# Kernel optimization log

Hardware: AMD Instinct MI355X
Metric: run time of the kernel (lower is better)

Reference implementation:

```python
import jax, jax.numpy as jnp
import numpy as np

D_MODEL = 1024
N_HEADS = 16
D_HEAD = D_MODEL // N_HEADS
B, T = 2, 2048


def setup_inputs() -> dict:
    key = jax.random.key(0)
    ks = jax.random.split(key, 8)
    s = 1.0 / np.sqrt(D_MODEL)
    return {
        "x": jax.random.normal(ks[0], (B, T, D_MODEL), dtype=jnp.float32),
        "ln_g": jnp.ones((D_MODEL,), jnp.float32),
        "ln_b": jnp.zeros((D_MODEL,), jnp.float32),
        "w_qkv": jax.random.normal(ks[1], (D_MODEL, 3 * D_MODEL), jnp.float32) * s,
        "b_qkv": jnp.zeros((3 * D_MODEL,), jnp.float32),
        "w_gate": jax.random.normal(ks[2], (D_MODEL, D_MODEL), jnp.float32) * s,
        "b_gate": jnp.zeros((D_MODEL,), jnp.float32),
        "w_proj": jax.random.normal(ks[3], (D_MODEL, D_MODEL), jnp.float32) * s,
        "b_proj": jnp.zeros((D_MODEL,), jnp.float32),
    }


def reference(x, ln_g, ln_b, w_qkv, b_qkv, w_gate, b_gate, w_proj, b_proj):
    Bb, Tt, Dd = x.shape
    H, dh = N_HEADS, D_HEAD

    # LayerNorm (eps=1e-5, torch default)
    mu = jnp.mean(x, axis=-1, keepdims=True)
    var = jnp.mean((x - mu) ** 2, axis=-1, keepdims=True)
    x_norm = (x - mu) / jnp.sqrt(var + 1e-5) * ln_g + ln_b

    qkv = x_norm @ w_qkv + b_qkv
    q, k, v = jnp.split(qkv, 3, axis=-1)

    # concept gate on the RAW input x (not x_norm), normalized by its mean
    gate_sig = jax.nn.sigmoid(x @ w_gate + b_gate)
    gate_norm = gate_sig / (jnp.mean(gate_sig, axis=-1, keepdims=True) + 1e-5)
    q = q * gate_norm
    k = k * gate_norm

    # [B,T,D] -> [B,H,T,dh]
    def to_heads(t):
        return t.reshape(Bb, Tt, H, dh).transpose(0, 2, 1, 3)

    q, k, v = to_heads(q), to_heads(k), to_heads(v)

    q = jax.nn.elu(q) + 1.0
    k = jax.nn.elu(k) + 1.0

    # materialized outer-product cumsum (faithful to source formulation)
    kv = jnp.einsum("bhtd,bhtm->bhtdm", k, v)          # [B,H,T,dh,dh]
    kv_cumsum = jnp.cumsum(kv, axis=2)
    out_num = jnp.einsum("bhtd,bhtdm->bhtm", q, kv_cumsum)
    k_cumsum = jnp.cumsum(k, axis=2)
    out_den = jnp.einsum("bhtd,bhtd->bht", q, k_cumsum)[..., None] + 1e-5
    out = out_num / out_den                              # [B,H,T,dh]

    out = out.transpose(0, 2, 1, 3).reshape(Bb, Tt, Dd)
    return out @ w_proj + b_proj
```

## Files before the change

### kernel.cpp

```cpp
#include <hip/hip_runtime.h>
#include <math.h>

constexpr int D      = 1024;
constexpr int H      = 16;
constexpr int DH     = 64;
constexpr int Bb     = 2;
constexpr int T      = 2048;
constexpr int BT     = Bb * T;
constexpr int CHUNK  = 64;
constexpr int NC     = T / CHUNK;
constexpr int LS     = 72;

typedef __attribute__((ext_vector_type(8))) short bf16x8;
typedef __attribute__((ext_vector_type(4))) float f32x4;

#define GLOAD_LDS16(gp, lp) \
    __builtin_amdgcn_global_load_lds((const __attribute__((address_space(1))) void*)(gp), \
                                     (__attribute__((address_space(3))) void*)(lp), 16, 0, 0)

__device__ __forceinline__ short to_bf16(float f) {
    unsigned u = __float_as_uint(f);
    unsigned r = (u + 0x7fffu + ((u >> 16) & 1u)) >> 16;
    return (short)r;
}
__device__ __forceinline__ float bf2f(short s) {
    return __uint_as_float(((unsigned)(unsigned short)s) << 16);
}

__device__ __forceinline__ float block_sum_256(float v, float* sbuf) {
    #pragma unroll
    for (int off = 32; off > 0; off >>= 1) v += __shfl_down(v, off, 64);
    int lane = threadIdx.x & 63;
    int wid  = threadIdx.x >> 6;
    if (lane == 0) sbuf[wid] = v;
    __syncthreads();
    float r = (threadIdx.x < 4) ? sbuf[threadIdx.x] : 0.0f;
    r += __shfl_down(r, 2, 64);
    r += __shfl_down(r, 1, 64);
    if (threadIdx.x == 0) sbuf[0] = r;
    __syncthreads();
    float outv = sbuf[0];
    __syncthreads();
    return outv;
}

__device__ __forceinline__ float elu1(float x) {
    return x > 0.0f ? x + 1.0f : __expf(x);
}

__global__ __launch_bounds__(256) void pre_kernel(const float* __restrict__ x,
                                                  const float* __restrict__ g,
                                                  const float* __restrict__ b,
                                                  const float* __restrict__ wq,
                                                  const float* __restrict__ wg,
                                                  const float* __restrict__ wp,
                                                  short* __restrict__ ynb,
                                                  short* __restrict__ xbb,
                                                  short* __restrict__ wTcomb,
                                                  short* __restrict__ wTp,
                                                  float* __restrict__ gmean) {
    __shared__ float sbuf[4];
    __shared__ short tile[32][33];
    int bid = blockIdx.x;
    if (bid < BT) {
        int row = bid;
        if (threadIdx.x == 0) gmean[row] = 0.0f;
        const float* xr = x + (size_t)row * D;
        int c = threadIdx.x * 4;
        float4 xv = *(const float4*)(xr + c);
        float mu = block_sum_256(xv.x + xv.y + xv.z + xv.w, sbuf) * (1.0f / D);
        float d0 = xv.x - mu, d1 = xv.y - mu, d2 = xv.z - mu, d3 = xv.w - mu;
        float var = block_sum_256(d0*d0 + d1*d1 + d2*d2 + d3*d3, sbuf) * (1.0f / D);
        float rstd = rsqrtf(var + 1e-5f);
        float4 gv = *(const float4*)(g + c);
        float4 bv = *(const float4*)(b + c);
        short4 o, xo;
        o.x = to_bf16(d0 * rstd * gv.x + bv.x);
        o.y = to_bf16(d1 * rstd * gv.y + bv.y);
        o.z = to_bf16(d2 * rstd * gv.z + bv.z);
        o.w = to_bf16(d3 * rstd * gv.w + bv.w);
        xo.x = to_bf16(xv.x); xo.y = to_bf16(xv.y);
        xo.z = to_bf16(xv.z); xo.w = to_bf16(xv.w);
        *(short4*)(ynb + (size_t)row * D + c) = o;
        *(short4*)(xbb + (size_t)row * D + c) = xo;
    } else {
        int t2 = bid - BT;
        const float* W; short* Wt; int N; int t;
        if (t2 < 3072)      { W = wq; Wt = wTcomb;                       N = 3072; t = t2; }
        else if (t2 < 4096) { W = wg; Wt = wTcomb + (size_t)3072 * 1024; N = 1024; t = t2 - 3072; }
        else                { W = wp; Wt = wTp;                          N = 1024; t = t2 - 4096; }
        int ntiles = N >> 5;
        int nb = (t % ntiles) * 32, kb = (t / ntiles) * 32;
        int tx = threadIdx.x & 31, ty = threadIdx.x >> 5;
        #pragma unroll
        for (int i = 0; i < 4; ++i) {
            int k = kb + ty + i * 8;
            tile[ty + i * 8][tx] = to_bf16(W[(size_t)k * N + nb + tx]);
        }
        __syncthreads();
        #pragma unroll
        for (int i = 0; i < 4; ++i) {
            int n = nb + ty + i * 8;
            Wt[(size_t)n * 1024 + kb + tx] = tile[tx][ty + i * 8];
        }
    }
}

#define SWZ(os) ((os) ^ ((((os) >> 6) & 3) << 3))
#define BARX() __builtin_amdgcn_s_barrier()
#define LGKM0() asm volatile("s_waitcnt lgkmcnt(0)" ::: "memory")
#define VMW(n) asm volatile("s_waitcnt vmcnt(" #n ")" ::: "memory")
#define MEMFENCE() asm volatile("" ::: "memory")

#define STG(Mp, rb, t, kc, isB) do {                                                       \
    short* _b = ldsbuf + ((((t) & 1)) << 15) + (((((isB) << 1) | (kc))) << 13) + wid * 1024; \
    const short* _g = (Mp) + (size_t)((rb) + wid * 32 + s_r) * 1024 + (t) * 64 + (kc) * 32 + s_c; \
    GLOAD_LDS16(_g, _b);                                                                   \
    GLOAD_LDS16(_g + (size_t)16 * 1024, _b + 512);                                         \
} while (0)

#define FRAGA(t, kc, mi) (*(const bf16x8*)(ldsbuf + (((t) & 1) << 15) + ((kc) << 13) + \
    SWZ((wm * 128 + (mi) * 16 + fr) * 32 + fk)))
#define FRAGB(t, kc, ni) (*(const bf16x8*)(ldsbuf + (((t) & 1) << 15) + ((2 + (kc)) << 13) + \
    SWZ((wn * 64 + (ni) * 16 + fr) * 32 + fk)))

#define GROUP(t, S1, S2, S3, S4, W2, W4) do {                                              \
    bf16x8 af[8], bq[4];                                                                   \
                                                                    \
    _Pragma("unroll") for (int mi = 0; mi < 8; ++mi) af[mi] = FRAGA(t, 0, mi);             \
    bq[0] = FRAGB(t, 0, 0); bq[1] = FRAGB(t, 0, 1);                                        \
    if (S1) STG(Wt, col0, (t) + 1, 1, 1);                                                  \
    BARX(); LGKM0();                                                                       \
    __builtin_amdgcn_s_setprio(1);                                                         \
    _Pragma("unroll") for (int mi = 0; mi < 8; ++mi) {                                     \
        acc[mi][0] = __builtin_amdgcn_mfma_f32_16x16x32_bf16(af[mi], bq[0], acc[mi][0], 0, 0, 0); \
        acc[mi][1] = __builtin_amdgcn_mfma_f32_16x16x32_bf16(af[mi], bq[1], acc[mi][1], 0, 0, 0); \
    }                                                                                      \
    __builtin_amdgcn_s_setprio(0);                                                         \
    BARX();                                                                                \
                                                                    \
    bq[2] = FRAGB(t, 0, 2); bq[3] = FRAGB(t, 0, 3);                                        \
    if (S2) STG(Ap, row0, (t) + 2, 0, 0);                                                  \
    BARX(); LGKM0();                                                                       \
    __builtin_amdgcn_s_setprio(1);                                                         \
    _Pragma("unroll") for (int mi = 0; mi < 8; ++mi) {                                     \
        acc[mi][2] = __builtin_amdgcn_mfma_f32_16x16x32_bf16(af[mi], bq[2], acc[mi][2], 0, 0, 0); \
        acc[mi][3] = __builtin_amdgcn_mfma_f32_16x16x32_bf16(af[mi], bq[3], acc[mi][3], 0, 0, 0); \
    }                                                                                      \
    __builtin_amdgcn_s_setprio(0);                                                         \
    W2; BARX();                                                                            \
                                                                    \
    _Pragma("unroll") for (int mi = 0; mi < 8; ++mi) af[mi] = FRAGA(t, 1, mi);             \
    bq[0] = FRAGB(t, 1, 0); bq[1] = FRAGB(t, 1, 1);                                        \
    if (S3) STG(Wt, col0, (t) + 2, 0, 1);                                                  \
    BARX(); LGKM0();                                                                       \
    __builtin_amdgcn_s_setprio(1);                                                         \
    _Pragma("unroll") for (int mi = 0; mi < 8; ++mi) {                                     \
        acc[mi][0] = __builtin_amdgcn_mfma_f32_16x16x32_bf16(af[mi], bq[0], acc[mi][0], 0, 0, 0); \
        acc[mi][1] = __builtin_amdgcn_mfma_f32_16x16x32_bf16(af[mi], bq[1], acc[mi][1], 0, 0, 0); \
    }                                                                                      \
    __builtin_amdgcn_s_setprio(0);                                                         \
    BARX();                                                                                \
                                                                    \
    bq[2] = FRAGB(t, 1, 2); bq[3] = FRAGB(t, 1, 3);                                        \
    if (S4) STG(Ap, row0, (t) + 2, 1, 0);                                                  \
    BARX(); LGKM0();                                                                       \
    __builtin_amdgcn_s_setprio(1);                                                         \
    _Pragma("unroll") for (int mi = 0; mi < 8; ++mi) {                                     \
        acc[mi][2] = __builtin_amdgcn_mfma_f32_16x16x32_bf16(af[mi], bq[2], acc[mi][2], 0, 0, 0); \
        acc[mi][3] = __builtin_amdgcn_mfma_f32_16x16x32_bf16(af[mi], bq[3], acc[mi][3], 0, 0, 0); \
    }                                                                                      \
    __builtin_amdgcn_s_setprio(0);                                                         \
    W4; BARX();                                                                            \
} while (0)

__global__ __launch_bounds__(512, 2) void gemm_fused_qkvgate(const short* __restrict__ xnb,
                                                             const short* __restrict__ xb,
                                                             const short* __restrict__ Wt,
                                                             const float* __restrict__ b_qkv,
                                                             const float* __restrict__ b_gate,
                                                             short* __restrict__ qkvb,
                                                             short* __restrict__ sigb,
                                                             float* __restrict__ gmean) {
    __shared__ short ldsbuf[2 * 32768];

    const int bid   = blockIdx.x;
    const int xcd   = bid & 7;
    const int local = bid >> 3;
    const int cx = xcd & 3, ry = xcd >> 2;
    const int bxx = cx * 4 + (local & 3);
    const int byy = ry * 8 + (local >> 2);
    const int row0 = byy * 256;
    const int col0 = bxx * 256;
    const bool isg = (col0 >= 3 * D);
    const short* Ap = isg ? xb : xnb;

    const int tid  = threadIdx.x;
    const int wid  = tid >> 6;
    const int lane = tid & 63;
    const int wm = wid >> 2;
    const int wn = wid & 3;
    const int fr = lane & 15;
    const int fk = (lane >> 4) * 8;

    const int s_r = lane >> 2;
    const int s_c = 8 * ((lane & 3) ^ ((lane >> 3) & 3));

    f32x4 acc[8][4] = {};

    STG(Ap, row0, 0, 0, 0); MEMFENCE();
    STG(Wt, col0, 0, 0, 1); MEMFENCE();
    STG(Ap, row0, 0, 1, 0); MEMFENCE();
    STG(Wt, col0, 0, 1, 1); MEMFENCE();
    STG(Ap, row0, 1, 0, 0); MEMFENCE();
    STG(Wt, col0, 1, 0, 1); MEMFENCE();
    STG(Ap, row0, 1, 1, 0);
    VMW(10);
    BARX();

    for (int t = 0; t < 14; ++t) GROUP(t, 1, 1, 1, 1, VMW(10), VMW(10));
    GROUP(14, 1, 0, 0, 0, VMW(8), VMW(4));
    GROUP(15, 0, 0, 0, 0, VMW(0), (void)0);

    const int ccol  = lane & 15;
    const int crow4 = (lane >> 4) * 4;
    if (!isg) {
        #pragma unroll
        for (int mi = 0; mi < 8; ++mi) {
            #pragma unroll
            for (int ni = 0; ni < 4; ++ni) {
                int col = col0 + wn * 64 + ni * 16 + ccol;
                float bv = b_qkv[col];
                #pragma unroll
                for (int r = 0; r < 4; ++r) {
                    int row = row0 + wm * 128 + mi * 16 + crow4 + r;
                    qkvb[(size_t)row * (3 * D) + col] = to_bf16(acc[mi][ni][r] + bv);
                }
            }
        }
    } else {
        #pragma unroll
        for (int mi = 0; mi < 8; ++mi) {
            #pragma unroll
            for (int r = 0; r < 4; ++r) {
                int lrow = row0 + wm * 128 + mi * 16 + crow4 + r;
                float psum = 0.0f;
                #pragma unroll
                for (int ni = 0; ni < 4; ++ni) {
                    int col = col0 + wn * 64 + ni * 16 + ccol - 3 * D;
                    float v = acc[mi][ni][r] + b_gate[col];
                    float sv = 1.0f / (1.0f + __expf(-v));
                    sigb[(size_t)lrow * D + col] = to_bf16(sv);
                    psum += sv;
                }
                psum += __shfl_xor(psum, 1, 64);
                psum += __shfl_xor(psum, 2, 64);
                psum += __shfl_xor(psum, 4, 64);
                psum += __shfl_xor(psum, 8, 64);
                if (ccol == 0) atomicAdd(&gmean[lrow], psum);
            }
        }
    }
}

__global__ __launch_bounds__(256) void chunk_state_mfma(const short* __restrict__ qkvb,
                                                        const short* __restrict__ sigb,
                                                        const float* __restrict__ gmean,
                                                        float* __restrict__ Sc,
                                                        float* __restrict__ zc) {
    __shared__ short Kt[DH * LS];
    __shared__ short Vt[DH * LS];
    int idx = blockIdx.x;
    int c = idx & (NC - 1), h = (idx >> 5) & (H - 1), b = idx >> 9;
    size_t bt0 = (size_t)b * T + c * CHUNK;
    const short* kbase = qkvb + bt0 * (3 * D) + D + h * DH;
    const short* vbase = kbase + D;
    const short* sbase = sigb + bt0 * D + h * DH;
    int tid = threadIdx.x;

    #pragma unroll
    for (int l = 0; l < 2; ++l) {
        int i  = tid + l * 256;
        int t  = i >> 3;
        int d8 = (i & 7) * 8;
        float invm = 1.0f / (gmean[bt0 + t] * (1.0f / D) + 1e-5f);
        bf16x8 kv = *(const bf16x8*)(kbase + (size_t)t * (3 * D) + d8);
        bf16x8 vv = *(const bf16x8*)(vbase + (size_t)t * (3 * D) + d8);
        bf16x8 sg = *(const bf16x8*)(sbase + (size_t)t * D + d8);
        #pragma unroll
        for (int j = 0; j < 8; ++j) {
            float gn = bf2f(sg[j]) * invm;
            Kt[(d8 + j) * LS + t] = to_bf16(elu1(bf2f(kv[j]) * gn));
            Vt[(d8 + j) * LS + t] = vv[j];
        }
    }
    __syncthreads();

    const int wv = tid >> 6, lane = tid & 63;
    const int fr = lane & 15, quad = lane >> 4;
    const int fk = quad * 8, crow4 = quad * 4, ccol = lane & 15;
    const int mbase = wv * 16;

    bf16x8 af[2];
    af[0] = *(const bf16x8*)&Vt[(mbase + fr) * LS + fk];
    af[1] = *(const bf16x8*)&Vt[(mbase + fr) * LS + 32 + fk];

    f32x4 acc[4] = {};
    #pragma unroll
    for (int n = 0; n < 4; ++n) {
        #pragma unroll
        for (int ck = 0; ck < 2; ++ck) {
            bf16x8 bk = *(const bf16x8*)&Kt[(n * 16 + fr) * LS + ck * 32 + fk];
            acc[n] = __builtin_amdgcn_mfma_f32_16x16x32_bf16(af[ck], bk, acc[n], 0, 0, 0);
        }
    }

    float* Sd = Sc + (size_t)idx * (DH * DH);
    #pragma unroll
    for (int n = 0; n < 4; ++n)
        #pragma unroll
        for (int r = 0; r < 4; ++r)
            Sd[(mbase + crow4 + r) * DH + n * 16 + ccol] = acc[n][r];

    if (tid < DH) {
        float zs = 0.0f;
        for (int t = 0; t < CHUNK; ++t) zs += bf2f(Kt[tid * LS + t]);
        zc[(size_t)idx * DH + tid] = zs;
    }
}

__global__ __launch_bounds__(256) void chunk_prefix_kernel(const float* __restrict__ S,
                                                           short* __restrict__ Spb,
                                                           float* __restrict__ z) {
    int bh   = blockIdx.x >> 4;
    int part = blockIdx.x & 15;
    int e    = part * 256 + threadIdx.x;
    const float* Sb = S + (size_t)bh * NC * DH * DH;
    short* Pb = Spb + (size_t)bh * NC * DH * DH;
    float acc = 0.0f;
    for (int c = 0; c < NC; ++c) {
        size_t off = (size_t)c * DH * DH + e;
        float t = Sb[off];
        Pb[off] = to_bf16(acc);
        acc += t;
    }
    if (part == 0 && threadIdx.x < DH) {
        float* zb = z + (size_t)bh * NC * DH;
        float za = 0.0f;
        for (int c = 0; c < NC; ++c) {
            float* p = zb + c * DH + threadIdx.x;
            float t = *p; *p = za; za += t;
        }
    }
}

__global__ __launch_bounds__(256) void chunk_attn_mfma(const short* __restrict__ qkvb,
                                                       const short* __restrict__ sigb,
                                                       const float* __restrict__ gmean,
                                                       const short* __restrict__ Spb,
                                                       const float* __restrict__ zc,
                                                       short* __restrict__ attnb) {
    __shared__ short Qs[CHUNK * LS];
    __shared__ short Ks[CHUNK * LS];
    __shared__ short Vt[DH * LS];
    __shared__ short Ss[DH * LS];
    __shared__ float zpL[DH];
    __shared__ float den[CHUNK];
    short* As = Ks;

    int idx = blockIdx.x;
    int c = idx & (NC - 1), h = (idx >> 5) & (H - 1), b = idx >> 9;
    size_t bt0 = (size_t)b * T + c * CHUNK;
    const short* qbase = qkvb + bt0 * (3 * D) + h * DH;
    const short* kbase = qbase + D;
    const short* vbase = qbase + 2 * D;
    const short* sbase = sigb + bt0 * D + h * DH;
    const short* spb = Spb + (size_t)idx * (DH * DH);
    int tid = threadIdx.x;

    #pragma unroll
    for (int l = 0; l < 2; ++l) {
        int i  = tid + l * 256;
        int t  = i >> 3;
        int d8 = (i & 7) * 8;
        float invm = 1.0f / (gmean[bt0 + t] * (1.0f / D) + 1e-5f);
        bf16x8 qv = *(const bf16x8*)(qbase + (size_t)t * (3 * D) + d8);
        bf16x8 kv = *(const bf16x8*)(kbase + (size_t)t * (3 * D) + d8);
        bf16x8 vv = *(const bf16x8*)(vbase + (size_t)t * (3 * D) + d8);
        bf16x8 sg = *(const bf16x8*)(sbase + (size_t)t * D + d8);
        bf16x8 qg, kg;
        #pragma unroll
        for (int j = 0; j < 8; ++j) {
            float gn = bf2f(sg[j]) * invm;
            qg[j] = to_bf16(elu1(bf2f(qv[j]) * gn));
            kg[j] = to_bf16(elu1(bf2f(kv[j]) * gn));
            Vt[(d8 + j) * LS + t] = vv[j];
        }
        *(bf16x8*)&Qs[t * LS + d8] = qg;
        *(bf16x8*)&Ks[t * LS + d8] = kg;
        *(bf16x8*)&Ss[t * LS + d8] = *(const bf16x8*)(spb + (size_t)i * 8);
    }
    if (tid < DH) zpL[tid] = zc[(size_t)idx * DH + tid];
    __syncthreads();

    const int wv = tid >> 6, lane = tid & 63;
    const int fr = lane & 15, quad = lane >> 4;
    const int fk = quad * 8, crow4 = quad * 4, ccol = lane & 15;
    const int tbase = wv * 16;

    bf16x8 aq[2];
    aq[0] = *(const bf16x8*)&Qs[(tbase + fr) * LS + fk];
    aq[1] = *(const bf16x8*)&Qs[(tbase + fr) * LS + 32 + fk];

    f32x4 accs[4] = {};
    #pragma unroll
    for (int n = 0; n < 4; ++n) {
        #pragma unroll
        for (int ck = 0; ck < 2; ++ck) {
            bf16x8 bk = *(const bf16x8*)&Ks[(n * 16 + fr) * LS + ck * 32 + fk];
            accs[n] = __builtin_amdgcn_mfma_f32_16x16x32_bf16(aq[ck], bk, accs[n], 0, 0, 0);
        }
    }
    __syncthreads();

    float part[4] = {0.f, 0.f, 0.f, 0.f};
    #pragma unroll
    for (int n = 0; n < 4; ++n) {
        #pragma unroll
        for (int r = 0; r < 4; ++r) {
            int tt = tbase + crow4 + r;
            int ss = n * 16 + ccol;
            float v = (ss <= tt) ? accs[n][r] : 0.0f;
            part[r] += v;
            As[tt * LS + ss] = to_bf16(v);
        }
    }
    #pragma unroll
    for (int r = 0; r < 4; ++r) {
        part[r] += __shfl_xor(part[r], 1, 64);
        part[r] += __shfl_xor(part[r], 2, 64);
        part[r] += __shfl_xor(part[r], 4, 64);
        part[r] += __shfl_xor(part[r], 8, 64);
    }
    if (fr == 0) {
        #pragma unroll
        for (int r = 0; r < 4; ++r) den[tbase + crow4 + r] = part[r];
    }
    __syncthreads();

    if (tid < CHUNK) {
        float qz = 0.0f;
        #pragma unroll 8
        for (int d = 0; d < DH; ++d) qz += bf2f(Qs[tid * LS + d]) * zpL[d];
        den[tid] += qz + 1e-5f;
    }

    f32x4 acco[4] = {};
    #pragma unroll
    for (int m4 = 0; m4 < 4; ++m4) {
        #pragma unroll
        for (int ck = 0; ck < 2; ++ck) {
            bf16x8 bs = *(const bf16x8*)&Ss[(m4 * 16 + fr) * LS + ck * 32 + fk];
            acco[m4] = __builtin_amdgcn_mfma_f32_16x16x32_bf16(aq[ck], bs, acco[m4], 0, 0, 0);
        }
    }
    bf16x8 aa[2];
    aa[0] = *(const bf16x8*)&As[(tbase + fr) * LS + fk];
    aa[1] = *(const bf16x8*)&As[(tbase + fr) * LS + 32 + fk];
    #pragma unroll
    for (int m4 = 0; m4 < 4; ++m4) {
        #pragma unroll
        for (int ck = 0; ck < 2; ++ck) {
            bf16x8 bv = *(const bf16x8*)&Vt[(m4 * 16 + fr) * LS + ck * 32 + fk];
            acco[m4] = __builtin_amdgcn_mfma_f32_16x16x32_bf16(aa[ck], bv, acco[m4], 0, 0, 0);
        }
    }
    __syncthreads();

    short* obase = attnb + bt0 * D + h * DH;
    #pragma unroll
    for (int r = 0; r < 4; ++r) {
        int tt = tbase + crow4 + r;
        float rv = 1.0f / den[tt];
        #pragma unroll
        for (int m4 = 0; m4 < 4; ++m4)
            obase[(size_t)tt * D + m4 * 16 + ccol] = to_bf16(acco[m4][r] * rv);
    }
}

__global__ __launch_bounds__(256) void gemm_proj64(const short* __restrict__ A,
                                                   const short* __restrict__ Bt,
                                                   const float* __restrict__ bias,
                                                   float* __restrict__ C) {
    constexpr int BK = 32, K = 1024, N = 1024;
    __shared__ short Als[64 * BK];
    __shared__ short Bls[128 * BK];

    const int bid   = blockIdx.x;
    const int xcd   = bid & 7;
    const int local = bid >> 3;
    const int cx = xcd & 3, ry = xcd >> 2;
    const int lx = local & 1, ly = local >> 1;
    const int bxx = cx * 2 + lx;
    const int byy = ry * 32 + ly;

    const int tid  = threadIdx.x;
    const int wave = tid >> 6;
    const int lane = tid & 63;
    const int row0 = byy * 64;
    const int col0 = bxx * 128;
    const int wn = wave * 32;

    f32x4 acc[4][2] = {};
    const int srow = lane >> 2;
    const int skk  = (lane & 3) * 8;
    const int fr = lane & 15;
    const int fk = (lane >> 4) * 8;

    for (int k0 = 0; k0 < K; k0 += BK) {
        __syncthreads();
        #pragma unroll
        for (int u = 0; u < 3; ++u) {
            int cc = wave * 3 + u;
            if (cc < 4) {
                int r = cc * 16 + srow;
                GLOAD_LDS16(A + (size_t)(row0 + r) * K + k0 + skk, &Als[cc * 512]);
            } else {
                int c2 = cc - 4;
                int r = c2 * 16 + srow;
                GLOAD_LDS16(Bt + (size_t)(col0 + r) * K + k0 + skk, &Bls[c2 * 512]);
            }
        }
        __syncthreads();

        bf16x8 af[4], bfr[2];
        #pragma unroll
        for (int i = 0; i < 4; ++i)
            af[i] = *(const bf16x8*)&Als[(i * 16 + fr) * BK + fk];
        #pragma unroll
        for (int j = 0; j < 2; ++j)
            bfr[j] = *(const bf16x8*)&Bls[(wn + j * 16 + fr) * BK + fk];
        #pragma unroll
        for (int mi = 0; mi < 4; ++mi)
            #pragma unroll
            for (int ni = 0; ni < 2; ++ni)
                acc[mi][ni] = __builtin_amdgcn_mfma_f32_16x16x32_bf16(af[mi], bfr[ni], acc[mi][ni], 0, 0, 0);
    }

    const int ccol  = lane & 15;
    const int crow4 = (lane >> 4) * 4;
    #pragma unroll
    for (int mi = 0; mi < 4; ++mi) {
        #pragma unroll
        for (int ni = 0; ni < 2; ++ni) {
            int col = col0 + wn + ni * 16 + ccol;
            float bv = bias[col];
            #pragma unroll
            for (int r = 0; r < 4; ++r) {
                int row = row0 + mi * 16 + crow4 + r;
                C[(size_t)row * N + col] = acc[mi][ni][r] + bv;
            }
        }
    }
}

extern "C" void kernel_launch(void* const* d_in, const int* in_sizes, int n_in,
                              void* d_out, int out_size, void* d_ws, size_t ws_size,
                              hipStream_t stream) {
    const float* x      = (const float*)d_in[0];
    const float* ln_g   = (const float*)d_in[1];
    const float* ln_b   = (const float*)d_in[2];
    const float* w_qkv  = (const float*)d_in[3];
    const float* b_qkv  = (const float*)d_in[4];
    const float* w_gate = (const float*)d_in[5];
    const float* b_gate = (const float*)d_in[6];
    const float* w_proj = (const float*)d_in[7];
    const float* b_proj = (const float*)d_in[8];
    float* out = (float*)d_out;

    short* xnb   = (short*)d_ws;
    short* xb    = xnb + (size_t)BT * D;
    short* wTc   = xb + (size_t)BT * D;
    short* wTp   = wTc + (size_t)4096 * 1024;
    short* qkvb  = wTp + (size_t)D * D;
    short* sigb  = qkvb + (size_t)BT * 3 * D;
    short* attnb = sigb + (size_t)BT * D;
    float* zc    = (float*)(attnb + (size_t)BT * D);
    float* gmean = zc + (size_t)Bb * H * NC * DH;
    float* Sc    = (float*)xnb;
    short* Spb   = wTc;

    pre_kernel<<<BT + 5120, 256, 0, stream>>>(x, ln_g, ln_b, w_qkv, w_gate, w_proj,
                                              xnb, xb, wTc, wTp, gmean);
    gemm_fused_qkvgate<<<256, 512, 0, stream>>>(
        xnb, xb, wTc, b_qkv, b_gate, qkvb, sigb, gmean);
    chunk_state_mfma<<<Bb * H * NC, 256, 0, stream>>>(qkvb, sigb, gmean, Sc, zc);
    chunk_prefix_kernel<<<Bb * H * 16, 256, 0, stream>>>(Sc, Spb, zc);
    chunk_attn_mfma<<<Bb * H * NC, 256, 0, stream>>>(qkvb, sigb, gmean, Spb, zc, attnb);
    gemm_proj64<<<512, 256, 0, stream>>>(attnb, wTp, b_proj, out);
}
```

Measured before the change: 191.2 us.

## Use wave-per-row LayerNorm and parallelize small serial reductions across threads

LayerNorm now assigns one wavefront per row (four rows per block) and uses shuffle-only reductions, removing block-level syncs and shrinking the grid. The column sums in chunk_state and the q·z denominator in chunk_attn now split each row across four lanes with vector LDS loads and a shuffle reduction, instead of 64 threads looping serially. The prefix kernel preloads all chunk values into registers before the scan so the loads can be issued together. Together these trim latency in several small phases, at the cost of more registers in the prefix kernel.

New measurement: 190.6 us. No clear change (-0.3%).

```diff
diff --git a/kernel.cpp b/kernel.cpp
--- a/kernel.cpp
+++ b/kernel.cpp
@@ -25,23 +25,6 @@
 }
 __device__ __forceinline__ float bf2f(short s) {
     return __uint_as_float(((unsigned)(unsigned short)s) << 16);
-}
-
-__device__ __forceinline__ float block_sum_256(float v, float* sbuf) {
-    #pragma unroll
-    for (int off = 32; off > 0; off >>= 1) v += __shfl_down(v, off, 64);
-    int lane = threadIdx.x & 63;
-    int wid  = threadIdx.x >> 6;
-    if (lane == 0) sbuf[wid] = v;
-    __syncthreads();
-    float r = (threadIdx.x < 4) ? sbuf[threadIdx.x] : 0.0f;
-    r += __shfl_down(r, 2, 64);
-    r += __shfl_down(r, 1, 64);
-    if (threadIdx.x == 0) sbuf[0] = r;
-    __syncthreads();
-    float outv = sbuf[0];
-    __syncthreads();
-    return outv;
 }
 
 __device__ __forceinline__ float elu1(float x) {
@@ -59,32 +42,50 @@
                                                   short* __restrict__ wTcomb,
                                                   short* __restrict__ wTp,
                                                   float* __restrict__ gmean) {
-    __shared__ float sbuf[4];
     __shared__ short tile[32][33];
     int bid = blockIdx.x;
-    if (bid < BT) {
-        int row = bid;
-        if (threadIdx.x == 0) gmean[row] = 0.0f;
+    if (bid < 1024) {
+        int row  = bid * 4 + (threadIdx.x >> 6);
+        int lane = threadIdx.x & 63;
         const float* xr = x + (size_t)row * D;
-        int c = threadIdx.x * 4;
-        float4 xv = *(const float4*)(xr + c);
-        float mu = block_sum_256(xv.x + xv.y + xv.z + xv.w, sbuf) * (1.0f / D);
-        float d0 = xv.x - mu, d1 = xv.y - mu, d2 = xv.z - mu, d3 = xv.w - mu;
-        float var = block_sum_256(d0*d0 + d1*d1 + d2*d2 + d3*d3, sbuf) * (1.0f / D);
-        float rstd = rsqrtf(var + 1e-5f);
-        float4 gv = *(const float4*)(g + c);
-        float4 bv = *(const float4*)(b + c);
-        short4 o, xo;
-        o.x = to_bf16(d0 * rstd * gv.x + bv.x);
-        o.y = to_bf16(d1 * rstd * gv.y + bv.y);
-        o.z = to_bf16(d2 * rstd * gv.z + bv.z);
-        o.w = to_bf16(d3 * rstd * gv.w + bv.w);
-        xo.x = to_bf16(xv.x); xo.y = to_bf16(xv.y);
-        xo.z = to_bf16(xv.z); xo.w = to_bf16(xv.w);
-        *(short4*)(ynb + (size_t)row * D + c) = o;
-        *(short4*)(xbb + (size_t)row * D + c) = xo;
+        float4 xv[4];
+        float s = 0.0f;
+        #pragma unroll
+        for (int i = 0; i < 4; ++i) {
+            xv[i] = *(const float4*)(xr + i * 256 + lane * 4);
+            s += xv[i].x + xv[i].y + xv[i].z + xv[i].w;
+        }
+        #pragma unroll
+        for (int off = 32; off > 0; off >>= 1) s += __shfl_xor(s, off, 64);
+        float mu = s * (1.0f / D);
+        float vs = 0.0f;
+        #pragma unroll
+        for (int i = 0; i < 4; ++i) {
+            float d0 = xv[i].x - mu, d1 = xv[i].y - mu;
+            float d2 = xv[i].z - mu, d3 = xv[i].w - mu;
+            vs += d0 * d0 + d1 * d1 + d2 * d2 + d3 * d3;
+        }
+        #pragma unroll
+        for (int off = 32; off > 0; off >>= 1) vs += __shfl_xor(vs, off, 64);
+        float rstd = rsqrtf(vs * (1.0f / D) + 1e-5f);
+        if (lane == 0) gmean[row] = 0.0f;
+        #pragma unroll
+        for (int i = 0; i < 4; ++i) {
+            int cc = i * 256 + lane * 4;
+            float4 gv = *(const float4*)(g + cc);
+            float4 bv = *(const float4*)(b + cc);
+            short4 o, xo;
+            o.x = to_bf16((xv[i].x - mu) * rstd * gv.x + bv.x);
+            o.y = to_bf16((xv[i].y - mu) * rstd * gv.y + bv.y);
+            o.z = to_bf16((xv[i].z - mu) * rstd * gv.z + bv.z);
+            o.w = to_bf16((xv[i].w - mu) * rstd * gv.w + bv.w);
+            xo.x = to_bf16(xv[i].x); xo.y = to_bf16(xv[i].y);
+            xo.z = to_bf16(xv[i].z); xo.w = to_bf16(xv[i].w);
+            *(short4*)(ynb + (size_t)row * D + cc) = o;
+            *(short4*)(xbb + (size_t)row * D + cc) = xo;
+        }
     } else {
-        int t2 = bid - BT;
+        int t2 = bid - 1024;
         const float* W; short* Wt; int N; int t;
         if (t2 < 3072)      { W = wq; Wt = wTcomb;                       N = 3072; t = t2; }
         else if (t2 < 4096) { W = wg; Wt = wTcomb + (size_t)3072 * 1024; N = 1024; t = t2 - 3072; }
@@ -126,7 +127,6 @@
 
 #define GROUP(t, S1, S2, S3, S4, W2, W4) do {                                              \
     bf16x8 af[8], bq[4];                                                                   \
-                                                                    \
     _Pragma("unroll") for (int mi = 0; mi < 8; ++mi) af[mi] = FRAGA(t, 0, mi);             \
     bq[0] = FRAGB(t, 0, 0); bq[1] = FRAGB(t, 0, 1);                                        \
     if (S1) STG(Wt, col0, (t) + 1, 1, 1);                                                  \
@@ -138,7 +138,6 @@
     }                                                                                      \
     __builtin_amdgcn_s_setprio(0);                                                         \
     BARX();                                                                                \
-                                                                    \
     bq[2] = FRAGB(t, 0, 2); bq[3] = FRAGB(t, 0, 3);                                        \
     if (S2) STG(Ap, row0, (t) + 2, 0, 0);                                                  \
     BARX(); LGKM0();                                                                       \
@@ -149,7 +148,6 @@
     }                                                                                      \
     __builtin_amdgcn_s_setprio(0);                                                         \
     W2; BARX();                                                                            \
-                                                                    \
     _Pragma("unroll") for (int mi = 0; mi < 8; ++mi) af[mi] = FRAGA(t, 1, mi);             \
     bq[0] = FRAGB(t, 1, 0); bq[1] = FRAGB(t, 1, 1);                                        \
     if (S3) STG(Wt, col0, (t) + 2, 0, 1);                                                  \
@@ -161,7 +159,6 @@
     }                                                                                      \
     __builtin_amdgcn_s_setprio(0);                                                         \
     BARX();                                                                                \
-                                                                    \
     bq[2] = FRAGB(t, 1, 2); bq[3] = FRAGB(t, 1, 3);                                        \
     if (S4) STG(Ap, row0, (t) + 2, 1, 0);                                                  \
     BARX(); LGKM0();                                                                       \
@@ -322,10 +319,16 @@
         for (int r = 0; r < 4; ++r)
             Sd[(mbase + crow4 + r) * DH + n * 16 + ccol] = acc[n][r];
 
-    if (tid < DH) {
+    {
+        int d = tid >> 2, p = tid & 3;
+        bf16x8 k0 = *(const bf16x8*)&Kt[d * LS + p * 16];
+        bf16x8 k1 = *(const bf16x8*)&Kt[d * LS + p * 16 + 8];
         float zs = 0.0f;
-        for (int t = 0; t < CHUNK; ++t) zs += bf2f(Kt[tid * LS + t]);
-        zc[(size_t)idx * DH + tid] = zs;
+        #pragma unroll
+        for (int j = 0; j < 8; ++j) zs += bf2f(k0[j]) + bf2f(k1[j]);
+        zs += __shfl_xor(zs, 1, 64);
+        zs += __shfl_xor(zs, 2, 64);
+        if (p == 0) zc[(size_t)idx * DH + d] = zs;
     }
 }
 
@@ -337,19 +340,25 @@
     int e    = part * 256 + threadIdx.x;
     const float* Sb = S + (size_t)bh * NC * DH * DH;
     short* Pb = Spb + (size_t)bh * NC * DH * DH;
+    float v[NC];
+    #pragma unroll
+    for (int c = 0; c < NC; ++c) v[c] = Sb[(size_t)c * DH * DH + e];
     float acc = 0.0f;
+    #pragma unroll
     for (int c = 0; c < NC; ++c) {
-        size_t off = (size_t)c * DH * DH + e;
-        float t = Sb[off];
-        Pb[off] = to_bf16(acc);
-        acc += t;
+        Pb[(size_t)c * DH * DH + e] = to_bf16(acc);
+        acc += v[c];
     }
     if (part == 0 && threadIdx.x < DH) {
-        float* zb = z + (size_t)bh * NC * DH;
+        float* zb = z + (size_t)bh * NC * DH + threadIdx.x;
+        float zv[NC];
+        #pragma unroll
+        for (int c = 0; c < NC; ++c) zv[c] = zb[(size_t)c * DH];
         float za = 0.0f;
+        #pragma unroll
         for (int c = 0; c < NC; ++c) {
-            float* p = zb + c * DH + threadIdx.x;
-            float t = *p; *p = za; za += t;
+            zb[(size_t)c * DH] = za;
+            za += zv[c];
         }
     }
 }
@@ -448,11 +457,17 @@
     }
     __syncthreads();
 
-    if (tid < CHUNK) {
+    {
+        int t = tid >> 2, p = tid & 3;
+        bf16x8 q0 = *(const bf16x8*)&Qs[t * LS + p * 16];
+        bf16x8 q1 = *(const bf16x8*)&Qs[t * LS + p * 16 + 8];
         float qz = 0.0f;
-        #pragma unroll 8
-        for (int d = 0; d < DH; ++d) qz += bf2f(Qs[tid * LS + d]) * zpL[d];
-        den[tid] += qz + 1e-5f;
+        #pragma unroll
+        for (int j = 0; j < 8; ++j)
+            qz += bf2f(q0[j]) * zpL[p * 16 + j] + bf2f(q1[j]) * zpL[p * 16 + 8 + j];
+        qz += __shfl_xor(qz, 1, 64);
+        qz += __shfl_xor(qz, 2, 64);
+        if (p == 0) den[t] += qz + 1e-5f;
     }
 
     f32x4 acco[4] = {};
@@ -590,8 +605,8 @@
     float* Sc    = (float*)xnb;
     short* Spb   = wTc;
 
-    pre_kernel<<<BT + 5120, 256, 0, stream>>>(x, ln_g, ln_b, w_qkv, w_gate, w_proj,
-                                              xnb, xb, wTc, wTp, gmean);
+    pre_kernel<<<1024 + 5120, 256, 0, stream>>>(x, ln_g, ln_b, w_qkv, w_gate, w_proj,
+                                                xnb, xb, wTc, wTp, gmean);
     gemm_fused_qkvgate<<<256, 512, 0, stream>>>(
         xnb, xb, wTc, b_qkv, b_gate, qkvb, sigb, gmean);
     chunk_state_mfma<<<Bb * H * NC, 256, 0, stream>>>(qkvb, sigb, gmean, Sc, zc);
```
